# Performance work log

Measured on AMD Instinct MI355X. Metric: run time of the kernel, lower is better.

Reference implementation:

```python
import jax, jax.numpy as jnp
import numpy as np

TOP_K = 2


def setup_inputs() -> dict:
    key = jax.random.key(0)
    ks = jax.random.split(key, 9)
    T, D, E, F, FS = 8192, 2048, 8, 1024, 2048
    s = lambda k, shape, fan: jax.random.normal(k, shape, jnp.float32) * (fan ** -0.5)
    return {
        'hidden_states': jax.random.normal(ks[0], (T, D), jnp.float32),
        'gate_w': s(ks[1], (D, E), D),
        'w_gate': s(ks[2], (E, D, F), D),
        'w_up': s(ks[3], (E, D, F), D),
        'w_down': s(ks[4], (E, F, D), F),
        'ws_gate': s(ks[5], (D, FS), D),
        'ws_up': s(ks[6], (D, FS), D),
        'ws_down': s(ks[7], (FS, D), FS),
        'wsg': s(ks[8], (D, 1), D),
    }


def reference(hidden_states, gate_w, w_gate, w_up, w_down, ws_gate, ws_up, ws_down, wsg):
    E = gate_w.shape[1]
    h = hidden_states  # [T, D]
    # Router: softmax in fp32, top-k, normalized top-k probs
    logits = h @ gate_w  # [T, E]
    probs = jax.nn.softmax(logits.astype(jnp.float32), axis=-1)
    topk_w, topk_i = jax.lax.top_k(probs, TOP_K)  # [T, K]
    topk_w = topk_w / jnp.sum(topk_w, axis=-1, keepdims=True)
    topk_w = topk_w.astype(h.dtype)
    # Dense combine weights [T, E]: weight of expert e for each token (0 if not routed)
    comb = jnp.sum(jax.nn.one_hot(topk_i, E, dtype=topk_w.dtype) * topk_w[..., None], axis=1)
    # Per-expert gated MLP, weighted combine (zero weight == token not dispatched)
    out = jnp.zeros_like(h)
    for e in range(E):
        act = jax.nn.silu(h @ w_gate[e]) * (h @ w_up[e])  # [T, F]
        out = out + comb[:, e:e + 1] * (act @ w_down[e])
    # Shared expert with sigmoid gate
    shared = (jax.nn.silu(h @ ws_gate) * (h @ ws_up)) @ ws_down
    out = out + jax.nn.sigmoid(h @ wsg) * shared
    return out.astype(hidden_states.dtype)
```

## Files before the change

### kernel.cpp

```cpp
#include <hip/hip_runtime.h>
#include <hip/hip_bf16.h>

typedef short bf16x8 __attribute__((ext_vector_type(8)));
typedef float f32x4 __attribute__((ext_vector_type(4)));

__device__ __forceinline__ unsigned short f2b(float f) {
  union { float f; unsigned u; } v; v.f = f;
  unsigned r = v.u + 0x7FFF + ((v.u >> 16) & 1);
  return (unsigned short)(r >> 16);
}

__device__ __forceinline__ float b2f(unsigned short u) {
  union { unsigned u; float f; } v; v.u = ((unsigned)u) << 16;
  return v.f;
}

__device__ __forceinline__ void async_b128(const void* g, void* l) {
  __builtin_amdgcn_global_load_lds(
      (const __attribute__((address_space(1))) unsigned int*)g,
      (__attribute__((address_space(3))) unsigned int*)l, 16, 0, 0);
}

__global__ void zero_f32_kernel(float* __restrict__ p, long n) {
  long i = (long)blockIdx.x * blockDim.x + threadIdx.x;
  long stride = (long)gridDim.x * blockDim.x;
  for (; i < n; i += stride) p[i] = 0.f;
}
__global__ void zero_i32_kernel(int* __restrict__ p, int n) {
  int i = blockIdx.x * blockDim.x + threadIdx.x;
  if (i < n) p[i] = 0;
}

__global__ __launch_bounds__(256) void convert_bf16_kernel(
    const float* __restrict__ src, unsigned short* __restrict__ dst, long n8) {
  long i = (long)blockIdx.x * blockDim.x + threadIdx.x;
  long stride = (long)gridDim.x * blockDim.x;
  for (; i < n8; i += stride) {
    const float* s = src + i * 8;
    float4 v0 = *(const float4*)s;
    float4 v1 = *(const float4*)(s + 4);
    bf16x8 w;
    w[0] = (short)f2b(v0.x); w[1] = (short)f2b(v0.y); w[2] = (short)f2b(v0.z); w[3] = (short)f2b(v0.w);
    w[4] = (short)f2b(v1.x); w[5] = (short)f2b(v1.y); w[6] = (short)f2b(v1.z); w[7] = (short)f2b(v1.w);
    *(bf16x8*)(dst + i * 8) = w;
  }
}

__global__ __launch_bounds__(256) void transpose_convert_kernel(
    const float* __restrict__ srcAll, unsigned short* __restrict__ dstAll,
    int R, int C) {
  const float* src = srcAll + (size_t)blockIdx.z * R * C;
  unsigned short* dst = dstAll + (size_t)blockIdx.z * R * C;
  int c0 = blockIdx.x * 64, r0 = blockIdx.y * 64;
  __shared__ float tile[64][73];
  int t = threadIdx.x;
  int sr = t >> 3;
  int sc = (t & 7) * 8;
#pragma unroll
  for (int rr = 0; rr < 2; ++rr) {
    int row = sr + rr * 32;
    const float* s = src + (size_t)(r0 + row) * C + c0 + sc;
    float4 v0 = *(const float4*)s;
    float4 v1 = *(const float4*)(s + 4);
    tile[row][sc + 0] = v0.x; tile[row][sc + 1] = v0.y;
    tile[row][sc + 2] = v0.z; tile[row][sc + 3] = v0.w;
    tile[row][sc + 4] = v1.x; tile[row][sc + 5] = v1.y;
    tile[row][sc + 6] = v1.z; tile[row][sc + 7] = v1.w;
  }
  __syncthreads();
#pragma unroll
  for (int pp = 0; pp < 2; ++pp) {
    int cc = sr + pp * 32;
    int rc = sc;
    bf16x8 w;
#pragma unroll
    for (int j = 0; j < 8; ++j) w[j] = (short)f2b(tile[rc + j][cc]);
    *(bf16x8*)(dst + (size_t)(c0 + cc) * R + r0 + rc) = w;
  }
}

__global__ __launch_bounds__(64) void router_kernel(
    const float* __restrict__ h, const float* __restrict__ gate_w,
    const float* __restrict__ wsg,
    int* __restrict__ cnt, int* __restrict__ slot_e, int* __restrict__ slot_pos,
    float* __restrict__ slot_w, float* __restrict__ gout, int D) {
  int t = blockIdx.x;
  int lane = threadIdx.x;
  float acc[8] = {0.f, 0.f, 0.f, 0.f, 0.f, 0.f, 0.f, 0.f};
  float aw = 0.f;
  const float* hrow = h + (size_t)t * D;
  for (int d = lane; d < D; d += 64) {
    float hv = hrow[d];
    float4 g0 = *(const float4*)(gate_w + (size_t)d * 8);
    float4 g1 = *(const float4*)(gate_w + (size_t)d * 8 + 4);
    acc[0] += hv * g0.x; acc[1] += hv * g0.y; acc[2] += hv * g0.z; acc[3] += hv * g0.w;
    acc[4] += hv * g1.x; acc[5] += hv * g1.y; acc[6] += hv * g1.z; acc[7] += hv * g1.w;
    aw += hv * wsg[d];
  }
#pragma unroll
  for (int off = 32; off > 0; off >>= 1) {
#pragma unroll
    for (int e = 0; e < 8; ++e) acc[e] += __shfl_down(acc[e], off);
    aw += __shfl_down(aw, off);
  }
  if (lane == 0) {
    int e0 = 0; float m0v = acc[0];
#pragma unroll
    for (int e = 1; e < 8; ++e) if (acc[e] > m0v) { m0v = acc[e]; e0 = e; }
    int e1 = -1; float m1v = -3.4e38f;
#pragma unroll
    for (int e = 0; e < 8; ++e) if (e != e0 && acc[e] > m1v) { m1v = acc[e]; e1 = e; }
    if (e1 < 0) e1 = (e0 + 1) & 7;
    float r = __expf(m1v - m0v);
    float w0 = 1.f / (1.f + r);
    float w1 = 1.f - w0;
    int p;
    p = atomicAdd(&cnt[e0], 1);
    slot_e[2 * t] = e0; slot_pos[2 * t] = p; slot_w[2 * t] = w0;
    p = atomicAdd(&cnt[e1], 1);
    slot_e[2 * t + 1] = e1; slot_pos[2 * t + 1] = p; slot_w[2 * t + 1] = w1;
    gout[t] = 1.f / (1.f + __expf(-aw));
  }
}

__global__ void scan_kernel(const int* __restrict__ cnt, int* __restrict__ offs, int E) {
  if (threadIdx.x == 0 && blockIdx.x == 0) {
    int s = 0;
    for (int e = 0; e < E; ++e) { offs[e] = s; s += cnt[e]; }
    offs[E] = s;
  }
}

__global__ void fill_kernel(const int* __restrict__ slot_e, const int* __restrict__ slot_pos,
                            const float* __restrict__ slot_w, const int* __restrict__ offs,
                            int* __restrict__ rowtok, float* __restrict__ roww,
                            int* __restrict__ tokslot, int n2T, int E) {
  int i = blockIdx.x * blockDim.x + threadIdx.x;
  if (i < n2T) {
    int e = slot_e[i];
    if (e < 0) e = 0; if (e >= E) e = E - 1;
    int row = offs[e] + slot_pos[i];
    if (row < 0) row = 0; if (row >= n2T) row = n2T - 1;
    rowtok[row] = i >> 1;
    roww[row] = slot_w[i];
    tokslot[i] = row;
  }
}

#define LDSOFF(row, kg) (((row) >> 3) * 512 + (kg) * 64 + ((row) & 7) * 8)

template <bool EXPERT, int K>
__global__ __launch_bounds__(256) void gemm_act3_kernel(
    const unsigned short* __restrict__ hb,
    const unsigned short* __restrict__ BgT,
    const unsigned short* __restrict__ BuT,
    unsigned short* __restrict__ actOut,
    const int* __restrict__ offs, const int* __restrict__ rowtok,
    int N, int rowsDirect, int T) {
  int e = EXPERT ? blockIdx.z : 0;
  int base = 0, cnt = rowsDirect;
  if (EXPERT) { base = offs[e]; cnt = offs[e + 1] - base; }
  int m0 = blockIdx.x * 128;
  if (m0 >= cnt) return;
  int n0 = blockIdx.y * 64;

  const unsigned short* Bg = BgT + (size_t)e * N * K;
  const unsigned short* Bu = BuT + (size_t)e * N * K;

  __shared__ __align__(16) unsigned short As[128 * 64];
  __shared__ __align__(16) unsigned short Bgs[64 * 64];
  __shared__ __align__(16) unsigned short Bus[64 * 64];

  int tid = threadIdx.x, lane = tid & 63, wave = tid >> 6;
  int r8 = lane & 7, kg = lane >> 3;
  int quad = lane >> 4, l16 = lane & 15;

  const unsigned short* aSrc[4];
#pragma unroll
  for (int t = 0; t < 4; ++t) {
    int gr = m0 + wave * 32 + t * 8 + r8;
    if (gr >= cnt) gr = cnt - 1;
    int tok = EXPERT ? rowtok[base + gr] : gr;
    if (tok < 0) tok = 0; if (tok >= T) tok = T - 1;
    aSrc[t] = hb + (size_t)tok * K + kg * 8;
  }
  const unsigned short* gSrc[2];
  const unsigned short* uSrc[2];
#pragma unroll
  for (int t = 0; t < 2; ++t) {
    int n = n0 + wave * 16 + t * 8 + r8;
    gSrc[t] = Bg + (size_t)n * K + kg * 8;
    uSrc[t] = Bu + (size_t)n * K + kg * 8;
  }
  unsigned short* aDst[4];
  unsigned short* gDst[2];
  unsigned short* uDst[2];
#pragma unroll
  for (int t = 0; t < 4; ++t) aDst[t] = As + (wave * 4 + t) * 512;
#pragma unroll
  for (int t = 0; t < 2; ++t) { gDst[t] = Bgs + (wave * 2 + t) * 512; uDst[t] = Bus + (wave * 2 + t) * 512; }

  f32x4 accG[2][4] = {};
  f32x4 accU[2][4] = {};

  for (int kt = 0; kt < K; kt += 64) {
#pragma unroll
    for (int t = 0; t < 4; ++t) async_b128(aSrc[t] + kt, aDst[t]);
#pragma unroll
    for (int t = 0; t < 2; ++t) { async_b128(gSrc[t] + kt, gDst[t]); async_b128(uSrc[t] + kt, uDst[t]); }
    __syncthreads();
#pragma unroll
    for (int ks = 0; ks < 2; ++ks) {
      int kq = ks * 4 + quad;
      bf16x8 a[2], bg[4], bu[4];
#pragma unroll
      for (int mi = 0; mi < 2; ++mi) {
        int m = wave * 32 + mi * 16 + l16;
        a[mi] = *(const bf16x8*)(As + LDSOFF(m, kq));
      }
#pragma unroll
      for (int nj = 0; nj < 4; ++nj) {
        int n = nj * 16 + l16;
        bg[nj] = *(const bf16x8*)(Bgs + LDSOFF(n, kq));
        bu[nj] = *(const bf16x8*)(Bus + LDSOFF(n, kq));
      }
#pragma unroll
      for (int mi = 0; mi < 2; ++mi)
#pragma unroll
        for (int nj = 0; nj < 4; ++nj) {
          accG[mi][nj] = __builtin_amdgcn_mfma_f32_16x16x32_bf16(a[mi], bg[nj], accG[mi][nj], 0, 0, 0);
          accU[mi][nj] = __builtin_amdgcn_mfma_f32_16x16x32_bf16(a[mi], bu[nj], accU[mi][nj], 0, 0, 0);
        }
    }
    __syncthreads();
  }

#pragma unroll
  for (int mi = 0; mi < 2; ++mi)
#pragma unroll
    for (int nj = 0; nj < 4; ++nj)
#pragma unroll
      for (int r = 0; r < 4; ++r) {
        int grow = m0 + wave * 32 + mi * 16 + quad * 4 + r;
        if (grow < cnt) {
          int col = n0 + nj * 16 + l16;
          float gv = accG[mi][nj][r], uv = accU[mi][nj][r];
          float sv = gv / (1.f + __expf(-gv)) * uv;
          actOut[(size_t)(base + grow) * N + col] = f2b(sv);
        }
      }
}

template <int MODE, int K>
__global__ __launch_bounds__(256) void gemm_comb3_kernel(
    const unsigned short* __restrict__ A,
    const unsigned short* __restrict__ BT,
    const int* __restrict__ offs,
    const int* __restrict__ tokslot,
    const float* __restrict__ slot_w,
    const float* __restrict__ gsig,
    const unsigned short* __restrict__ ye_in,
    unsigned short* __restrict__ ye_out,
    float* __restrict__ out,
    int N, int rowsDirect, int T) {
  int e = (MODE == 0) ? blockIdx.z : 0;
  int base = 0, cnt = rowsDirect;
  if (MODE == 0) { base = offs[e]; cnt = offs[e + 1] - base; }
  int m0 = blockIdx.x * 128;
  if (m0 >= cnt) return;
  int n0 = blockIdx.y * 128;

  const unsigned short* B = BT + (size_t)e * N * K;

  __shared__ __align__(16) unsigned short As[128 * 64];
  __shared__ __align__(16) unsigned short Bs[128 * 64];

  int tid = threadIdx.x, lane = tid & 63, wave = tid >> 6;
  int r8 = lane & 7, kg = lane >> 3;
  int quad = lane >> 4, l16 = lane & 15;
  int mBase = (wave >> 1) * 64, nBase = (wave & 1) * 64;

  const unsigned short* aSrc[4];
  const unsigned short* bSrc[4];
#pragma unroll
  for (int t = 0; t < 4; ++t) {
    int gr = m0 + wave * 32 + t * 8 + r8;
    if (gr >= cnt) gr = cnt - 1;
    aSrc[t] = A + (size_t)(base + gr) * K + kg * 8;
    int n = n0 + wave * 32 + t * 8 + r8;
    bSrc[t] = B + (size_t)n * K + kg * 8;
  }
  unsigned short* aDst[4];
  unsigned short* bDst[4];
#pragma unroll
  for (int t = 0; t < 4; ++t) {
    aDst[t] = As + (wave * 4 + t) * 512;
    bDst[t] = Bs + (wave * 4 + t) * 512;
  }

  f32x4 acc[4][4] = {};

  for (int kt = 0; kt < K; kt += 64) {
#pragma unroll
    for (int t = 0; t < 4; ++t) { async_b128(aSrc[t] + kt, aDst[t]); async_b128(bSrc[t] + kt, bDst[t]); }
    __syncthreads();
#pragma unroll
    for (int ks = 0; ks < 2; ++ks) {
      int kq = ks * 4 + quad;
      bf16x8 a[4], b[4];
#pragma unroll
      for (int mi = 0; mi < 4; ++mi) {
        int m = mBase + mi * 16 + l16;
        a[mi] = *(const bf16x8*)(As + LDSOFF(m, kq));
      }
#pragma unroll
      for (int nj = 0; nj < 4; ++nj) {
        int n = nBase + nj * 16 + l16;
        b[nj] = *(const bf16x8*)(Bs + LDSOFF(n, kq));
      }
#pragma unroll
      for (int mi = 0; mi < 4; ++mi)
#pragma unroll
        for (int nj = 0; nj < 4; ++nj)
          acc[mi][nj] = __builtin_amdgcn_mfma_f32_16x16x32_bf16(a[mi], b[nj], acc[mi][nj], 0, 0, 0);
    }
    __syncthreads();
  }

#pragma unroll
  for (int mi = 0; mi < 4; ++mi)
#pragma unroll
    for (int r = 0; r < 4; ++r) {
      int grow = m0 + mBase + mi * 16 + quad * 4 + r;
      if (grow < cnt) {
        if (MODE == 0) {
#pragma unroll
          for (int nj = 0; nj < 4; ++nj) {
            int col = n0 + nBase + nj * 16 + l16;
            ye_out[(size_t)(base + grow) * N + col] = f2b(acc[mi][nj][r]);
          }
        } else {
          int r0 = tokslot[2 * grow], r1 = tokslot[2 * grow + 1];
          float w0 = slot_w[2 * grow], w1 = slot_w[2 * grow + 1];
          float gv = gsig[grow];
#pragma unroll
          for (int nj = 0; nj < 4; ++nj) {
            int col = n0 + nBase + nj * 16 + l16;
            float v = acc[mi][nj][r];
            float e0 = b2f(ye_in[(size_t)r0 * N + col]);
            float e1 = b2f(ye_in[(size_t)r1 * N + col]);
            out[(size_t)grow * N + col] = gv * v + w0 * e0 + w1 * e1;
          }
        }
      }
    }
}

template <bool EXPERT>
__global__ __launch_bounds__(256) void gemm_act_f32_kernel(
    const float* __restrict__ X, const float* __restrict__ BgAll,
    const float* __restrict__ BuAll, unsigned short* __restrict__ actOut,
    const int* __restrict__ offs, const int* __restrict__ rowtok,
    int K, int N, int rowsDirect, int maxTok) {
  int e = EXPERT ? blockIdx.z : 0;
  int base = 0, cnt = rowsDirect;
  if (EXPERT) { base = offs[e]; cnt = offs[e + 1] - base; }
  int m0 = blockIdx.y * 64;
  if (m0 >= cnt) return;
  int n0 = blockIdx.x * 64;
  const float* Bg = BgAll + (size_t)e * K * N;
  const float* Bu = BuAll + (size_t)e * K * N;
  __shared__ __align__(16) short As[64][72];
  __shared__ __align__(16) short Bgs[64][72];
  __shared__ __align__(16) short Bus[64][72];
  int tid = threadIdx.x, lane = tid & 63, wave = tid >> 6;
  int quad = lane >> 4, l16 = lane & 15;
  int mBase = (wave >> 1) * 32, nBase = (wave & 1) * 32;
  f32x4 accG[2][2] = {};
  f32x4 accU[2][2] = {};
  int sr = tid >> 3, sc = (tid & 7) * 8;
  size_t aRowOff[2];
#pragma unroll
  for (int rr = 0; rr < 2; ++rr) {
    int gr = m0 + sr + rr * 32;
    if (gr >= cnt) gr = cnt - 1;
    int tokenRow = EXPERT ? rowtok[base + gr] : gr;
    if (tokenRow < 0) tokenRow = 0;
    if (tokenRow >= maxTok) tokenRow = maxTok - 1;
    aRowOff[rr] = (size_t)tokenRow * K;
  }
  for (int kt = 0; kt < K; kt += 64) {
#pragma unroll
    for (int rr = 0; rr < 2; ++rr) {
      int r = sr + rr * 32;
      const float* src = X + aRowOff[rr] + kt + sc;
      float4 v0 = *(const float4*)src;
      float4 v1 = *(const float4*)(src + 4);
      bf16x8 w;
      w[0] = (short)f2b(v0.x); w[1] = (short)f2b(v0.y); w[2] = (short)f2b(v0.z); w[3] = (short)f2b(v0.w);
      w[4] = (short)f2b(v1.x); w[5] = (short)f2b(v1.y); w[6] = (short)f2b(v1.z); w[7] = (short)f2b(v1.w);
      *(bf16x8*)&As[r][sc] = w;
    }
#pragma unroll
    for (int rr = 0; rr < 2; ++rr) {
      int kk = sr + rr * 32;
      const float* bg = Bg + (size_t)(kt + kk) * N + n0 + sc;
      const float* bu = Bu + (size_t)(kt + kk) * N + n0 + sc;
      float4 g0 = *(const float4*)bg; float4 g1 = *(const float4*)(bg + 4);
      float4 u0 = *(const float4*)bu; float4 u1 = *(const float4*)(bu + 4);
      Bgs[sc + 0][kk] = (short)f2b(g0.x); Bgs[sc + 1][kk] = (short)f2b(g0.y);
      Bgs[sc + 2][kk] = (short)f2b(g0.z); Bgs[sc + 3][kk] = (short)f2b(g0.w);
      Bgs[sc + 4][kk] = (short)f2b(g1.x); Bgs[sc + 5][kk] = (short)f2b(g1.y);
      Bgs[sc + 6][kk] = (short)f2b(g1.z); Bgs[sc + 7][kk] = (short)f2b(g1.w);
      Bus[sc + 0][kk] = (short)f2b(u0.x); Bus[sc + 1][kk] = (short)f2b(u0.y);
      Bus[sc + 2][kk] = (short)f2b(u0.z); Bus[sc + 3][kk] = (short)f2b(u0.w);
      Bus[sc + 4][kk] = (short)f2b(u1.x); Bus[sc + 5][kk] = (short)f2b(u1.y);
      Bus[sc + 6][kk] = (short)f2b(u1.z); Bus[sc + 7][kk] = (short)f2b(u1.w);
    }
    __syncthreads();
#pragma unroll
    for (int ks = 0; ks < 2; ++ks) {
      bf16x8 a[2], bg[2], bu[2];
#pragma unroll
      for (int i = 0; i < 2; ++i)
        a[i] = *(const bf16x8*)&As[mBase + i * 16 + l16][ks * 32 + quad * 8];
#pragma unroll
      for (int i = 0; i < 2; ++i) {
        bg[i] = *(const bf16x8*)&Bgs[nBase + i * 16 + l16][ks * 32 + quad * 8];
        bu[i] = *(const bf16x8*)&Bus[nBase + i * 16 + l16][ks * 32 + quad * 8];
      }
#pragma unroll
      for (int i = 0; i < 2; ++i)
#pragma unroll
        for (int j = 0; j < 2; ++j) {
          accG[i][j] = __builtin_amdgcn_mfma_f32_16x16x32_bf16(a[i], bg[j], accG[i][j], 0, 0, 0);
          accU[i][j] = __builtin_amdgcn_mfma_f32_16x16x32_bf16(a[i], bu[j], accU[i][j], 0, 0, 0);
        }
    }
    __syncthreads();
  }
#pragma unroll
  for (int i = 0; i < 2; ++i)
#pragma unroll
    for (int j = 0; j < 2; ++j)
#pragma unroll
      for (int r = 0; r < 4; ++r) {
        int row = mBase + i * 16 + quad * 4 + r;
        int grow = m0 + row;
        if (grow < cnt) {
          int col = n0 + nBase + j * 16 + l16;
          float gv = accG[i][j][r], uv = accU[i][j][r];
          float sv = gv / (1.f + __expf(-gv)) * uv;
          actOut[(size_t)(base + grow) * N + col] = f2b(sv);
        }
      }
}

template <int MODE>
__global__ __launch_bounds__(256) void gemm_comb_f32_kernel(
    const unsigned short* __restrict__ A, const float* __restrict__ BAll,
    const int* __restrict__ offs, const int* __restrict__ rowtok,
    const float* __restrict__ roww, float* __restrict__ accum,
    const float* __restrict__ gsig, float* __restrict__ out,
    int K, int N, int rowsDirect, int maxTok) {
  int e = (MODE == 0) ? blockIdx.z : 0;
  int base = 0, cnt = rowsDirect;
  if (MODE == 0) { base = offs[e]; cnt = offs[e + 1] - base; }
  int m0 = blockIdx.y * 64;
  if (m0 >= cnt) return;
  int n0 = blockIdx.x * 64;
  const float* B = BAll + (size_t)e * K * N;
  __shared__ __align__(16) short As[64][72];
  __shared__ __align__(16) short Bs[64][72];
  int tid = threadIdx.x, lane = tid & 63, wave = tid >> 6;
  int quad = lane >> 4, l16 = lane & 15;
  int mBase = (wave >> 1) * 32, nBase = (wave & 1) * 32;
  f32x4 acc[2][2] = {};
  int sr = tid >> 3, sc = (tid & 7) * 8;
  size_t aRowOff[2];
#pragma unroll
  for (int rr = 0; rr < 2; ++rr) {
    int gr = m0 + sr + rr * 32;
    if (gr >= cnt) gr = cnt - 1;
    aRowOff[rr] = (size_t)(base + gr) * K;
  }
  for (int kt = 0; kt < K; kt += 64) {
#pragma unroll
    for (int rr = 0; rr < 2; ++rr) {
      int r = sr + rr * 32;
      *(bf16x8*)&As[r][sc] = *(const bf16x8*)(A + aRowOff[rr] + kt + sc);
    }
#pragma unroll
    for (int rr = 0; rr < 2; ++rr) {
      int kk = sr + rr * 32;
      const float* bp = B + (size_t)(kt + kk) * N + n0 + sc;
      float4 b0 = *(const float4*)bp; float4 b1 = *(const float4*)(bp + 4);
      Bs[sc + 0][kk] = (short)f2b(b0.x); Bs[sc + 1][kk] = (short)f2b(b0.y);
      Bs[sc + 2][kk] = (short)f2b(b0.z); Bs[sc + 3][kk] = (short)f2b(b0.w);
      Bs[sc + 4][kk] = (short)f2b(b1.x); Bs[sc + 5][kk] = (short)f2b(b1.y);
      Bs[sc + 6][kk] = (short)f2b(b1.z); Bs[sc + 7][kk] = (short)f2b(b1.w);
    }
    __syncthreads();
#pragma unroll
    for (int ks = 0; ks < 2; ++ks) {
      bf16x8 a[2], b[2];
#pragma unroll
      for (int i = 0; i < 2; ++i)
        a[i] = *(const bf16x8*)&As[mBase + i * 16 + l16][ks * 32 + quad * 8];
#pragma unroll
      for (int i = 0; i < 2; ++i)
        b[i] = *(const bf16x8*)&Bs[nBase + i * 16 + l16][ks * 32 + quad * 8];
#pragma unroll
      for (int i = 0; i < 2; ++i)
#pragma unroll
        for (int j = 0; j < 2; ++j)
          acc[i][j] = __builtin_amdgcn_mfma_f32_16x16x32_bf16(a[i], b[j], acc[i][j], 0, 0, 0);
    }
    __syncthreads();
  }
#pragma unroll
  for (int i = 0; i < 2; ++i)
#pragma unroll
    for (int j = 0; j < 2; ++j)
#pragma unroll
      for (int r = 0; r < 4; ++r) {
        int row = mBase + i * 16 + quad * 4 + r;
        int grow = m0 + row;
        if (grow < cnt) {
          int col = n0 + nBase + j * 16 + l16;
          float v = acc[i][j][r];
          if (MODE == 0) {
            int tok = rowtok[base + grow];
            if (tok < 0) tok = 0;
            if (tok >= maxTok) tok = maxTok - 1;
            atomicAdd(&accum[(size_t)tok * N + col], roww[base + grow] * v);
          } else {
            out[(size_t)grow * N + col] = accum[(size_t)grow * N + col] + gsig[grow] * v;
          }
        }
      }
}

extern "C" void kernel_launch(void* const* d_in, const int* in_sizes, int n_in,
                              void* d_out, int out_size, void* d_ws, size_t ws_size,
                              hipStream_t stream) {
  const float* h       = (const float*)d_in[0];
  const float* gate_w  = (const float*)d_in[1];
  const float* w_gate  = (const float*)d_in[2];
  const float* w_up    = (const float*)d_in[3];
  const float* w_down  = (const float*)d_in[4];
  const float* ws_gate = (const float*)d_in[5];
  const float* ws_up   = (const float*)d_in[6];
  const float* ws_down = (const float*)d_in[7];
  const float* wsg     = (const float*)d_in[8];
  float* out = (float*)d_out;

  const int D  = in_sizes[8];
  const int T  = in_sizes[0] / D;
  const int E  = in_sizes[1] / D;
  const int F  = in_sizes[2] / (E * D);
  const int FS = in_sizes[5] / D;
  (void)n_in; (void)out_size;

  const int actPerTok = (2 * F > FS ? 2 * F : FS);

  size_t al = 256;
  auto rnd = [&](size_t b) { return (b + al - 1) & ~(al - 1); };
  size_t need = 0;
  need += rnd((size_t)T * D * 2);
  need += rnd((size_t)E * D * F * 2) * 3;
  need += rnd((size_t)D * FS * 2) * 3;
  need += rnd((size_t)T * actPerTok * 2);
  need += rnd((size_t)T * 4);
  need += rnd((size_t)E * 4) + rnd((size_t)(E + 1) * 4);
  need += rnd((size_t)2 * T * 4) * 6;

  bool shapeOK = (D == 2048 && F == 1024 && FS == 2048 && E == 8 && (T % 128) == 0);

  if (shapeOK && ws_size >= need) {
    char* ws = (char*)d_ws;
    size_t off = 0;
    auto alloc = [&](size_t bytes) -> void* { void* p = ws + off; off += rnd(bytes); return p; };
    unsigned short* hb   = (unsigned short*)alloc((size_t)T * D * 2);
    unsigned short* wgT  = (unsigned short*)alloc((size_t)E * D * F * 2);
    unsigned short* wuT  = (unsigned short*)alloc((size_t)E * D * F * 2);
    unsigned short* wdT  = (unsigned short*)alloc((size_t)E * D * F * 2);
    unsigned short* wsgT = (unsigned short*)alloc((size_t)D * FS * 2);
    unsigned short* wsuT = (unsigned short*)alloc((size_t)D * FS * 2);
    unsigned short* wsdT = (unsigned short*)alloc((size_t)D * FS * 2);
    unsigned short* act  = (unsigned short*)alloc((size_t)T * actPerTok * 2);
    float* g      = (float*)alloc((size_t)T * 4);
    int* cnt      = (int*)alloc((size_t)E * 4);
    int* offs     = (int*)alloc((size_t)(E + 1) * 4);
    int* slot_e   = (int*)alloc((size_t)2 * T * 4);
    int* slot_pos = (int*)alloc((size_t)2 * T * 4);
    float* slot_w = (float*)alloc((size_t)2 * T * 4);
    int* rowtok   = (int*)alloc((size_t)2 * T * 4);
    float* roww   = (float*)alloc((size_t)2 * T * 4);
    int* tokslot  = (int*)alloc((size_t)2 * T * 4);

    unsigned short* ye = wgT;

    zero_i32_kernel<<<1, 64, 0, stream>>>(cnt, E);

    convert_bf16_kernel<<<2048, 256, 0, stream>>>(h, hb, (long)T * D / 8);
    transpose_convert_kernel<<<dim3(F / 64, D / 64, E), 256, 0, stream>>>(w_gate, wgT, D, F);
    transpose_convert_kernel<<<dim3(F / 64, D / 64, E), 256, 0, stream>>>(w_up, wuT, D, F);
    transpose_convert_kernel<<<dim3(D / 64, F / 64, E), 256, 0, stream>>>(w_down, wdT, F, D);
    transpose_convert_kernel<<<dim3(FS / 64, D / 64, 1), 256, 0, stream>>>(ws_gate, wsgT, D, FS);
    transpose_convert_kernel<<<dim3(FS / 64, D / 64, 1), 256, 0, stream>>>(ws_up, wsuT, D, FS);
    transpose_convert_kernel<<<dim3(D / 64, FS / 64, 1), 256, 0, stream>>>(ws_down, wsdT, FS, D);

    router_kernel<<<T, 64, 0, stream>>>(h, gate_w, wsg, cnt, slot_e, slot_pos, slot_w, g, D);
    scan_kernel<<<1, 64, 0, stream>>>(cnt, offs, E);
    fill_kernel<<<(2 * T + 255) / 256, 256, 0, stream>>>(slot_e, slot_pos, slot_w, offs,
                                                         rowtok, roww, tokslot, 2 * T, E);

    int gxM = T / 128;
    gemm_act3_kernel<true, 2048><<<dim3(gxM, F / 64, E), 256, 0, stream>>>(
        hb, wgT, wuT, act, offs, rowtok, F, 0, T);
    gemm_comb3_kernel<0, 1024><<<dim3(gxM, D / 128, E), 256, 0, stream>>>(
        act, wdT, offs, nullptr, nullptr, nullptr, nullptr, ye, nullptr, D, 0, T);
    gemm_act3_kernel<false, 2048><<<dim3(gxM, FS / 64, 1), 256, 0, stream>>>(
        hb, wsgT, wsuT, act, nullptr, nullptr, FS, T, T);
    gemm_comb3_kernel<1, 2048><<<dim3(gxM, D / 128, 1), 256, 0, stream>>>(
        act, wsdT, nullptr, tokslot, slot_w, g, ye, nullptr, out, D, T, T);
    return;
  }

  size_t perTok = (size_t)D * 4 + (size_t)actPerTok * 2 + 4 + 48;
  size_t avail = ws_size > 4096 ? ws_size - 4096 : 0;
  long TcL = (long)(avail / (perTok + 8));
  int Tc = (int)(TcL > T ? T : TcL);
  Tc &= ~63;
  if (Tc < 64) Tc = 64;

  for (int t0 = 0; t0 < T; t0 += Tc) {
    int Tcur = (T - t0 < Tc) ? (T - t0) : Tc;
    const float* hC = h + (size_t)t0 * D;
    float* outC = out + (size_t)t0 * D;

    char* ws = (char*)d_ws;
    size_t off = 0;
    auto alloc = [&](size_t bytes) -> void* { void* p = ws + off; off += rnd(bytes); return p; };
    float* accum = (float*)alloc((size_t)Tc * D * sizeof(float));
    unsigned short* act = (unsigned short*)alloc((size_t)Tc * actPerTok * 2);
    float* g      = (float*)alloc((size_t)Tc * 4);
    int* cnt      = (int*)alloc((size_t)E * 4);
    int* offs     = (int*)alloc((size_t)(E + 1) * 4);
    int* slot_e   = (int*)alloc((size_t)2 * Tc * 4);
    int* slot_pos = (int*)alloc((size_t)2 * Tc * 4);
    float* slot_w = (float*)alloc((size_t)2 * Tc * 4);
    int* rowtok   = (int*)alloc((size_t)2 * Tc * 4);
    float* roww   = (float*)alloc((size_t)2 * Tc * 4);
    int* tokslot  = (int*)alloc((size_t)2 * Tc * 4);

    int gy = (Tcur + 63) / 64;

    zero_i32_kernel<<<1, 64, 0, stream>>>(cnt, E);
    zero_f32_kernel<<<1024, 256, 0, stream>>>(accum, (long)Tcur * D);

    router_kernel<<<Tcur, 64, 0, stream>>>(hC, gate_w, wsg, cnt, slot_e, slot_pos, slot_w, g, D);
    scan_kernel<<<1, 64, 0, stream>>>(cnt, offs, E);
    fill_kernel<<<(2 * Tcur + 255) / 256, 256, 0, stream>>>(slot_e, slot_pos, slot_w, offs,
                                                            rowtok, roww, tokslot, 2 * Tcur, E);
    gemm_act_f32_kernel<true><<<dim3(F / 64, gy, E), 256, 0, stream>>>(
        hC, w_gate, w_up, act, offs, rowtok, D, F, 0, Tcur);
    gemm_comb_f32_kernel<0><<<dim3(D / 64, gy, E), 256, 0, stream>>>(
        act, w_down, offs, rowtok, roww, accum, nullptr, nullptr, F, D, 0, Tcur);
    gemm_act_f32_kernel<false><<<dim3(FS / 64, gy, 1), 256, 0, stream>>>(
        hC, ws_gate, ws_up, act, nullptr, nullptr, D, FS, Tcur, Tcur);
    gemm_comb_f32_kernel<1><<<dim3(D / 64, gy, 1), 256, 0, stream>>>(
        act, ws_down, nullptr, nullptr, nullptr, accum, g, outC, FS, D, Tcur, Tcur);
  }
}
```

Measured before the change: 1.682 ms.

## Double-buffer LDS tiles in MoE GEMM kernels and widen expert grids

Both GEMM kernels now keep two LDS buffers. The global-to-LDS async copy of the next K tile is issued before computing on the current tile, which overlaps memory latency with MFMA work and removes one barrier per iteration. The expert-GEMM grids are also sized for 2T/128 row tiles; since each expert receives at most T rows, the extra blocks just exit early. The cost is double the LDS per block (64KB), which lowers the number of resident blocks per CU.

```diff
diff --git a/kernel.cpp b/kernel.cpp
--- a/kernel.cpp
+++ b/kernel.cpp
@@ -167,9 +167,9 @@
   const unsigned short* Bg = BgT + (size_t)e * N * K;
   const unsigned short* Bu = BuT + (size_t)e * N * K;
 
-  __shared__ __align__(16) unsigned short As[128 * 64];
-  __shared__ __align__(16) unsigned short Bgs[64 * 64];
-  __shared__ __align__(16) unsigned short Bus[64 * 64];
+  __shared__ __align__(16) unsigned short As[2][128 * 64];
+  __shared__ __align__(16) unsigned short Bgs[2][64 * 64];
+  __shared__ __align__(16) unsigned short Bus[2][64 * 64];
 
   int tid = threadIdx.x, lane = tid & 63, wave = tid >> 6;
   int r8 = lane & 7, kg = lane >> 3;
@@ -192,23 +192,25 @@
     gSrc[t] = Bg + (size_t)n * K + kg * 8;
     uSrc[t] = Bu + (size_t)n * K + kg * 8;
   }
-  unsigned short* aDst[4];
-  unsigned short* gDst[2];
-  unsigned short* uDst[2];
-#pragma unroll
-  for (int t = 0; t < 4; ++t) aDst[t] = As + (wave * 4 + t) * 512;
-#pragma unroll
-  for (int t = 0; t < 2; ++t) { gDst[t] = Bgs + (wave * 2 + t) * 512; uDst[t] = Bus + (wave * 2 + t) * 512; }
+
+  auto stage = [&](int buf, int kt) {
+#pragma unroll
+    for (int t = 0; t < 4; ++t) async_b128(aSrc[t] + kt, As[buf] + (wave * 4 + t) * 512);
+#pragma unroll
+    for (int t = 0; t < 2; ++t) {
+      async_b128(gSrc[t] + kt, Bgs[buf] + (wave * 2 + t) * 512);
+      async_b128(uSrc[t] + kt, Bus[buf] + (wave * 2 + t) * 512);
+    }
+  };
 
   f32x4 accG[2][4] = {};
   f32x4 accU[2][4] = {};
 
+  stage(0, 0);
+  __syncthreads();
+  int cur = 0;
   for (int kt = 0; kt < K; kt += 64) {
-#pragma unroll
-    for (int t = 0; t < 4; ++t) async_b128(aSrc[t] + kt, aDst[t]);
-#pragma unroll
-    for (int t = 0; t < 2; ++t) { async_b128(gSrc[t] + kt, gDst[t]); async_b128(uSrc[t] + kt, uDst[t]); }
-    __syncthreads();
+    if (kt + 64 < K) stage(cur ^ 1, kt + 64);
 #pragma unroll
     for (int ks = 0; ks < 2; ++ks) {
       int kq = ks * 4 + quad;
@@ -216,13 +218,13 @@
 #pragma unroll
       for (int mi = 0; mi < 2; ++mi) {
         int m = wave * 32 + mi * 16 + l16;
-        a[mi] = *(const bf16x8*)(As + LDSOFF(m, kq));
+        a[mi] = *(const bf16x8*)(As[cur] + LDSOFF(m, kq));
       }
 #pragma unroll
       for (int nj = 0; nj < 4; ++nj) {
         int n = nj * 16 + l16;
-        bg[nj] = *(const bf16x8*)(Bgs + LDSOFF(n, kq));
-        bu[nj] = *(const bf16x8*)(Bus + LDSOFF(n, kq));
+        bg[nj] = *(const bf16x8*)(Bgs[cur] + LDSOFF(n, kq));
+        bu[nj] = *(const bf16x8*)(Bus[cur] + LDSOFF(n, kq));
       }
 #pragma unroll
       for (int mi = 0; mi < 2; ++mi)
@@ -233,6 +235,7 @@
         }
     }
     __syncthreads();
+    cur ^= 1;
   }
 
 #pragma unroll
@@ -272,8 +275,8 @@
 
   const unsigned short* B = BT + (size_t)e * N * K;
 
-  __shared__ __align__(16) unsigned short As[128 * 64];
-  __shared__ __align__(16) unsigned short Bs[128 * 64];
+  __shared__ __align__(16) unsigned short As[2][128 * 64];
+  __shared__ __align__(16) unsigned short Bs[2][128 * 64];
 
   int tid = threadIdx.x, lane = tid & 63, wave = tid >> 6;
   int r8 = lane & 7, kg = lane >> 3;
@@ -290,20 +293,22 @@
     int n = n0 + wave * 32 + t * 8 + r8;
     bSrc[t] = B + (size_t)n * K + kg * 8;
   }
-  unsigned short* aDst[4];
-  unsigned short* bDst[4];
-#pragma unroll
-  for (int t = 0; t < 4; ++t) {
-    aDst[t] = As + (wave * 4 + t) * 512;
-    bDst[t] = Bs + (wave * 4 + t) * 512;
-  }
+
+  auto stage = [&](int buf, int kt) {
+#pragma unroll
+    for (int t = 0; t < 4; ++t) {
+      async_b128(aSrc[t] + kt, As[buf] + (wave * 4 + t) * 512);
+      async_b128(bSrc[t] + kt, Bs[buf] + (wave * 4 + t) * 512);
+    }
+  };
 
   f32x4 acc[4][4] = {};
 
+  stage(0, 0);
+  __syncthreads();
+  int cur = 0;
   for (int kt = 0; kt < K; kt += 64) {
-#pragma unroll
-    for (int t = 0; t < 4; ++t) { async_b128(aSrc[t] + kt, aDst[t]); async_b128(bSrc[t] + kt, bDst[t]); }
-    __syncthreads();
+    if (kt + 64 < K) stage(cur ^ 1, kt + 64);
 #pragma unroll
     for (int ks = 0; ks < 2; ++ks) {
       int kq = ks * 4 + quad;
@@ -311,12 +316,12 @@
 #pragma unroll
       for (int mi = 0; mi < 4; ++mi) {
         int m = mBase + mi * 16 + l16;
-        a[mi] = *(const bf16x8*)(As + LDSOFF(m, kq));
+        a[mi] = *(const bf16x8*)(As[cur] + LDSOFF(m, kq));
       }
 #pragma unroll
       for (int nj = 0; nj < 4; ++nj) {
         int n = nBase + nj * 16 + l16;
-        b[nj] = *(const bf16x8*)(Bs + LDSOFF(n, kq));
+        b[nj] = *(const bf16x8*)(Bs[cur] + LDSOFF(n, kq));
       }
 #pragma unroll
       for (int mi = 0; mi < 4; ++mi)
@@ -325,6 +330,7 @@
           acc[mi][nj] = __builtin_amdgcn_mfma_f32_16x16x32_bf16(a[mi], b[nj], acc[mi][nj], 0, 0, 0);
     }
     __syncthreads();
+    cur ^= 1;
   }
 
 #pragma unroll
@@ -616,14 +622,15 @@
     fill_kernel<<<(2 * T + 255) / 256, 256, 0, stream>>>(slot_e, slot_pos, slot_w, offs,
                                                          rowtok, roww, tokslot, 2 * T, E);
 
-    int gxM = T / 128;
-    gemm_act3_kernel<true, 2048><<<dim3(gxM, F / 64, E), 256, 0, stream>>>(
+    int gxE = (2 * T) / 128;
+    int gxS = T / 128;
+    gemm_act3_kernel<true, 2048><<<dim3(gxE, F / 64, E), 256, 0, stream>>>(
         hb, wgT, wuT, act, offs, rowtok, F, 0, T);
-    gemm_comb3_kernel<0, 1024><<<dim3(gxM, D / 128, E), 256, 0, stream>>>(
+    gemm_comb3_kernel<0, 1024><<<dim3(gxE, D / 128, E), 256, 0, stream>>>(
         act, wdT, offs, nullptr, nullptr, nullptr, nullptr, ye, nullptr, D, 0, T);
-    gemm_act3_kernel<false, 2048><<<dim3(gxM, FS / 64, 1), 256, 0, stream>>>(
+    gemm_act3_kernel<false, 2048><<<dim3(gxS, FS / 64, 1), 256, 0, stream>>>(
         hb, wsgT, wsuT, act, nullptr, nullptr, FS, T, T);
-    gemm_comb3_kernel<1, 2048><<<dim3(gxM, D / 128, 1), 256, 0, stream>>>(
+    gemm_comb3_kernel<1, 2048><<<dim3(gxS, D / 128, 1), 256, 0, stream>>>(
         act, wsdT, nullptr, tokslot, slot_w, g, ye, nullptr, out, D, T, T);
     return;
   }
```

New measurement: 1.725 ms. 2.5% more time.
